# Optimization experiments

Measured on AMD Instinct MI355X. Metric: run time of the kernel, lower is better.

## Reference

```python
import jax, jax.numpy as jnp
import numpy as np

B, L, D, H = 1, 2048, 3072, 24
Dh = D // H            # 128
MLP = 4 * D            # 12288
EPS = 1e-6


def setup_inputs() -> dict:
    key = jax.random.key(0)
    ks = jax.random.split(key, 10)
    n = lambda k, shape, s=1.0: jax.random.normal(k, shape, jnp.float32) * s
    W = 0.02  # weight init scale
    return {
        "img": n(ks[0], (B, L, D)),
        "vec": n(ks[1], (B, D)),
        "pe": n(ks[2], (1, 1, L, Dh // 2, 2, 2)),
        "mod_w": n(ks[3], (D, 3 * D), W),
        "mod_b": jnp.zeros((3 * D,), jnp.float32),
        "lin1_w": n(ks[4], (D, 3 * D + MLP), W),
        "lin1_b": jnp.zeros((3 * D + MLP,), jnp.float32),
        "lin2_w": n(ks[5], (D + MLP, D), W),
        "lin2_b": jnp.zeros((D,), jnp.float32),
        "q_scale": jnp.ones((Dh,), jnp.float32),
        "k_scale": jnp.ones((Dh,), jnp.float32),
    }


def _rms_norm(x, scale):
    return x * jax.lax.rsqrt(jnp.mean(x * x, axis=-1, keepdims=True) + EPS) * scale


def _apply_rope(x, pe):
    # x: [B,H,L,Dh]; pe: [1,1,L,Dh/2,2,2]
    xr = x.reshape(*x.shape[:-1], Dh // 2, 1, 2)
    out = pe[..., 0] * xr[..., 0] + pe[..., 1] * xr[..., 1]  # [B,H,L,Dh/2,2]
    return out.reshape(*x.shape[:-1], Dh)


def reference(img, vec, pe, mod_w, mod_b, lin1_w, lin1_b, lin2_w, lin2_b, q_scale, k_scale):
    # adaLN modulation (single): shift / scale / gate, each [B,1,D]
    mod = jax.nn.silu(vec) @ mod_w + mod_b
    shift, scale, gate = jnp.split(mod[:, None, :], 3, axis=-1)

    # pre-norm LayerNorm (no affine) + modulation
    mu = jnp.mean(img, axis=-1, keepdims=True)
    var = jnp.var(img, axis=-1, keepdims=True)
    x = (1.0 + scale) * ((img - mu) * jax.lax.rsqrt(var + EPS)) + shift

    # fused QKV + MLP projection
    proj = x @ lin1_w + lin1_b                     # [B,L,3D+MLP]
    qkv, mlp = proj[..., : 3 * D], proj[..., 3 * D :]

    # 'B L (K H D) -> K B H L D'
    qkv = qkv.reshape(B, L, 3, H, Dh).transpose(2, 0, 3, 1, 4)
    q, k, v = qkv[0], qkv[1], qkv[2]

    # per-head QK RMSNorm
    q = _rms_norm(q, q_scale)
    k = _rms_norm(k, k_scale)

    # RoPE
    q = _apply_rope(q, pe)
    k = _apply_rope(k, pe)

    # attention (scale = head_dim**-0.5)
    scores = jnp.einsum("bhqd,bhkd->bhqk", q, k) * (Dh ** -0.5)
    probs = jax.nn.softmax(scores, axis=-1)
    attn = jnp.einsum("bhqk,bhkd->bhqd", probs, v)
    attn = attn.transpose(0, 2, 1, 3).reshape(B, L, D)  # 'B H L D -> B L (H D)'

    # gated parallel MLP output + residual
    out = jnp.concatenate([attn, jax.nn.gelu(mlp, approximate=True)], axis=-1) @ lin2_w + lin2_b
    return img + gate * out
```

## Files before the change

### kernel.cpp

```cpp
#include <hip/hip_runtime.h>
#include <hip/hip_bf16.h>
#include <stdint.h>


#define DEV static __device__ __forceinline__

typedef __attribute__((ext_vector_type(4))) float f32x4;
typedef __attribute__((ext_vector_type(16))) float f32x16;
typedef __attribute__((ext_vector_type(8))) short s8v;

DEV unsigned short f2bf(float f) {
  union { float f; unsigned u; } v; v.f = f;
  unsigned r = v.u + 0x7fffu + ((v.u >> 16) & 1u);
  return (unsigned short)(r >> 16);
}
DEV float bf2f(unsigned short b) {
  union { unsigned u; float f; } v; v.u = ((unsigned)b) << 16; return v.f;
}
DEV unsigned pk2bf(float a, float b) {
  union { __hip_bfloat162 h; unsigned u; } v;
  v.h = __float22bfloat162_rn(make_float2(a, b));
  return v.u;
}

DEV void gl_lds16(const void* g, void* l) {
  __builtin_amdgcn_global_load_lds(
      (const __attribute__((address_space(1))) unsigned int*)(uintptr_t)g,
      (__attribute__((address_space(3))) unsigned int*)(uint32_t)(uintptr_t)l,
      16, 0, 0);
}

__global__ __launch_bounds__(256) void modvec_partial(
    const float* __restrict__ vec, const float* __restrict__ mod_w, float* __restrict__ part) {
  __shared__ float s[384];
  const int tid = threadIdx.x;
  const int i0 = blockIdx.y * 384;
  for (int i = tid; i < 384; i += 256) {
    float v = vec[i0 + i];
    s[i] = v / (1.f + __expf(-v));
  }
  __syncthreads();
  const int j = blockIdx.x * 256 + tid;
  float acc = 0.f;
#pragma unroll 8
  for (int i = 0; i < 384; ++i) acc += s[i] * mod_w[(size_t)(i0 + i) * 9216 + j];
  part[(size_t)blockIdx.y * 9216 + j] = acc;
}

__global__ __launch_bounds__(256) void modvec_reduce(
    const float* __restrict__ part, const float* __restrict__ mod_b, float* __restrict__ mod) {
  const int j = blockIdx.x * 256 + threadIdx.x;
  float a = mod_b[j];
#pragma unroll
  for (int y = 0; y < 8; ++y) a += part[(size_t)y * 9216 + j];
  mod[j] = a;
}

__global__ __launch_bounds__(256) void ln_mod_kernel(
    const float* __restrict__ img, const float* __restrict__ mod, unsigned short* __restrict__ x) {
  const int l = blockIdx.x, tid = threadIdx.x;
  const int wave = tid >> 6;
  const f32x4* row = (const f32x4*)(img + (size_t)l * 3072);
  f32x4 v[3];
  float s = 0.f, s2 = 0.f;
#pragma unroll
  for (int i = 0; i < 3; ++i) {
    v[i] = row[tid + i * 256];
#pragma unroll
    for (int c = 0; c < 4; ++c) { s += v[i][c]; s2 += v[i][c] * v[i][c]; }
  }
#pragma unroll
  for (int m = 1; m < 64; m <<= 1) { s += __shfl_xor(s, m); s2 += __shfl_xor(s2, m); }
  __shared__ float rs[4], rs2[4];
  if ((tid & 63) == 0) { rs[wave] = s; rs2[wave] = s2; }
  __syncthreads();
  s = rs[0] + rs[1] + rs[2] + rs[3];
  s2 = rs2[0] + rs2[1] + rs2[2] + rs2[3];
  const float mu = s * (1.f / 3072.f);
  const float var = s2 * (1.f / 3072.f) - mu * mu;
  const float inv = rsqrtf(var + 1e-6f);
#pragma unroll
  for (int i = 0; i < 3; ++i) {
    int d0 = (tid + i * 256) * 4;
    unsigned out[2];
    unsigned short o[4];
#pragma unroll
    for (int c = 0; c < 4; ++c) {
      int d = d0 + c;
      float val = (1.f + mod[3072 + d]) * ((v[i][c] - mu) * inv) + mod[d];
      o[c] = f2bf(val);
    }
    out[0] = o[0] | ((unsigned)o[1] << 16);
    out[1] = o[2] | ((unsigned)o[3] << 16);
    *(uint2*)(x + (size_t)l * 3072 + d0) = make_uint2(out[0], out[1]);
  }
}

__global__ __launch_bounds__(256) void transpose_kernel(
    const float* __restrict__ W, unsigned short* __restrict__ Wt, int K, int N) {
  __shared__ float t[64][65];
  const int k0 = blockIdx.x * 64, n0 = blockIdx.y * 64;
  const int tid = threadIdx.x;
#pragma unroll
  for (int it = 0; it < 4; ++it) {
    const int k = it * 16 + (tid >> 4), c4 = (tid & 15) * 4;
    f32x4 v = *(const f32x4*)&W[(size_t)(k0 + k) * N + n0 + c4];
    t[k][c4] = v[0]; t[k][c4 + 1] = v[1]; t[k][c4 + 2] = v[2]; t[k][c4 + 3] = v[3];
  }
  __syncthreads();
#pragma unroll
  for (int it = 0; it < 2; ++it) {
    const int idx = it * 256 + tid;
    const int n = idx >> 3, k8 = (idx & 7) * 8;
    s8v o;
#pragma unroll
    for (int e = 0; e < 8; ++e) o[e] = (short)f2bf(t[k8 + e][n]);
    *(s8v*)&Wt[(size_t)(n0 + n) * K + k0 + k8] = o;
  }
}

template <int EPI>
__global__ __launch_bounds__(512, 2) void gemm256_kernel(
    const unsigned short* __restrict__ A, const unsigned short* __restrict__ Bt,
    const float* __restrict__ bias, void* __restrict__ Cout, void* __restrict__ Cout2,
    int K, int N, int nTile, int nBN) {
  __shared__ unsigned short lds[65536];
  const int tid = threadIdx.x;
  const int lane = tid & 63, w = tid >> 6;
  const int wm = w >> 2, wn = w & 3;
  const int l15 = lane & 15, l4 = lane >> 4;

  int bid = blockIdx.x;
  const int nwg = gridDim.x;
  bid = (bid & 7) * (nwg >> 3) + (bid >> 3);
  const int bz = bid / (nBN << 3);
  const int rem = bid - bz * (nBN << 3);
  const int m0 = (rem & 7) << 8;
  const int n0 = (rem >> 3) << 8;
  const int kOff = bz * nTile * 64;

  const int sr = (w << 3) + (lane >> 3);
  const int skc = ((lane & 7) ^ (sr & 7)) << 3;
  const size_t aBase = (size_t)m0 * K + kOff;
  const size_t bBase = (size_t)n0 * K + kOff;

  const int xs0 = (l4 ^ (l15 & 7)) << 3;
  const int xs1 = ((4 + l4) ^ (l15 & 7)) << 3;
  int aRow[4], bRow[2];
#pragma unroll
  for (int i = 0; i < 4; ++i) aRow[i] = (wm * 64 + i * 16 + l15) * 64;
#pragma unroll
  for (int j = 0; j < 2; ++j) bRow[j] = (wn * 32 + j * 16 + l15) * 64;

  f32x4 acc[2][2][4][2];
#pragma unroll
  for (int mq = 0; mq < 2; ++mq)
#pragma unroll
    for (int nq = 0; nq < 2; ++nq)
#pragma unroll
      for (int i = 0; i < 4; ++i)
#pragma unroll
        for (int j = 0; j < 2; ++j) acc[mq][nq][i][j] = (f32x4){0.f, 0.f, 0.f, 0.f};

#define STAGE(op, h, par, kt)                                                        \
  do {                                                                               \
    const unsigned short* _s = (op) ? Bt : A;                                        \
    const size_t _b = (op) ? bBase : aBase;                                          \
    unsigned short* _d = &lds[((par) << 15) + ((op) << 14) + ((h) << 13) + (w << 9)];\
    gl_lds16(_s + _b + (size_t)((h) * 128 + sr) * K + (kt) * 64 + skc, _d);          \
    gl_lds16(_s + _b + (size_t)((h) * 128 + 64 + sr) * K + (kt) * 64 + skc, _d + 4096);\
  } while (0)

#define FRAGP(op, h, par, rowoff, xsv) \
  (*(const s8v*)&lds[((par) << 15) + ((op) << 14) + ((h) << 13) + (rowoff) + (xsv)])

#define RD_A(dst, h, par)                                                       \
  _Pragma("unroll") for (int i = 0; i < 4; ++i) {                               \
    dst[i][0] = FRAGP(0, h, par, aRow[i], xs0);                                 \
    dst[i][1] = FRAGP(0, h, par, aRow[i], xs1);                                 \
  }

#define RD_B(dst, h, par)                                                       \
  _Pragma("unroll") for (int j = 0; j < 2; ++j) {                               \
    dst[j][0] = FRAGP(1, h, par, bRow[j], xs0);                                 \
    dst[j][1] = FRAGP(1, h, par, bRow[j], xs1);                                 \
  }

#define PH_OPEN()                                           \
  __builtin_amdgcn_s_barrier();                             \
  asm volatile("s_waitcnt lgkmcnt(0)" ::: "memory");        \
  __builtin_amdgcn_sched_barrier(0);                        \
  __builtin_amdgcn_s_setprio(1)

#define PH_CLOSE()                                          \
  __builtin_amdgcn_sched_barrier(0);                        \
  __builtin_amdgcn_s_setprio(0);                            \
  __builtin_amdgcn_s_barrier()

#define PH_CLOSE_VM(NN)                                     \
  __builtin_amdgcn_sched_barrier(0);                        \
  __builtin_amdgcn_s_setprio(0);                            \
  asm volatile("s_waitcnt vmcnt(" #NN ")" ::: "memory");    \
  __builtin_amdgcn_s_barrier()

#define MFMA_QUAD(mq, nq, av, bv)                                                      \
  _Pragma("unroll") for (int i = 0; i < 4; ++i) _Pragma("unroll") for (int j = 0; j < 2; ++j) { \
    acc[mq][nq][i][j] =                                                                \
        __builtin_amdgcn_mfma_f32_16x16x32_bf16(av[i][0], bv[j][0], acc[mq][nq][i][j], 0, 0, 0); \
    acc[mq][nq][i][j] =                                                                \
        __builtin_amdgcn_mfma_f32_16x16x32_bf16(av[i][1], bv[j][1], acc[mq][nq][i][j], 0, 0, 0); \
  }

  STAGE(0, 0, 0, 0); STAGE(1, 0, 0, 0); STAGE(1, 1, 0, 0); STAGE(0, 1, 0, 0);
  {
    const int k1 = (nTile > 1) ? 1 : 0;
    STAGE(0, 0, 1, k1); STAGE(1, 0, 1, k1); STAGE(1, 1, 1, k1);
  }
  asm volatile("s_waitcnt vmcnt(6)" ::: "memory");
  __builtin_amdgcn_s_barrier();

  s8v aA[4][2], aB[4][2], b0[2][2], b1[2][2];
  RD_A(aA, 0, 0);
  RD_B(b0, 0, 0);

#pragma unroll 2
  for (int t = 0; t < nTile; ++t) {
    const int p = t & 1, pn = p ^ 1;
    const int kt1 = (t + 1 < nTile) ? t + 1 : 0;
    const int kt2 = (t + 2 < nTile) ? t + 2 : 0;
    STAGE(0, 1, pn, kt1);
    PH_OPEN();
    RD_B(b1, 1, p);
    MFMA_QUAD(0, 0, aA, b0);
    PH_CLOSE();
    STAGE(0, 0, p, kt2);
    PH_OPEN();
    RD_A(aB, 1, p);
    MFMA_QUAD(0, 1, aA, b1);
    PH_CLOSE_VM(8);
    STAGE(1, 0, p, kt2);
    PH_OPEN();
    RD_A(aA, 0, pn);
    MFMA_QUAD(1, 0, aB, b0);
    PH_CLOSE_VM(8);
    STAGE(1, 1, p, kt2);
    PH_OPEN();
    RD_B(b0, 0, pn);
    MFMA_QUAD(1, 1, aB, b1);
    PH_CLOSE_VM(6);
  }

  asm volatile("s_waitcnt vmcnt(0) lgkmcnt(0)" ::: "memory");
  __builtin_amdgcn_s_barrier();

  if (EPI == 0) {
    if (n0 < 9216) {
#pragma unroll
      for (int mq = 0; mq < 2; ++mq)
#pragma unroll
        for (int nq = 0; nq < 2; ++nq)
#pragma unroll
          for (int j = 0; j < 2; ++j) {
            const int col = n0 + nq * 128 + wn * 32 + j * 16 + l15;
            const float bj = bias[col];
#pragma unroll
            for (int i = 0; i < 4; ++i) {
              const int row0 = m0 + mq * 128 + wm * 64 + i * 16 + (l4 << 2);
#pragma unroll
              for (int r = 0; r < 4; ++r)
                ((unsigned short*)Cout)[(size_t)(row0 + r) * 9216 + col] =
                    f2bf(acc[mq][nq][i][j][r] + bj);
            }
          }
    } else {
#pragma unroll
      for (int mq = 0; mq < 2; ++mq)
#pragma unroll
        for (int nq = 0; nq < 2; ++nq)
#pragma unroll
          for (int j = 0; j < 2; ++j) {
            const int col = n0 + nq * 128 + wn * 32 + j * 16 + l15;
            const float bj = bias[col];
#pragma unroll
            for (int i = 0; i < 4; ++i) {
              const int row0 = m0 + mq * 128 + wm * 64 + i * 16 + (l4 << 2);
#pragma unroll
              for (int r = 0; r < 4; ++r) {
                const float v = acc[mq][nq][i][j][r] + bj;
                const float y = 0.7978845608f * (v + 0.044715f * v * v * v);
                const float ex = exp2f(2.8853900818f * y);
                const float g = v - v * __builtin_amdgcn_rcpf(ex + 1.f);
                ((unsigned short*)Cout2)[(size_t)(row0 + r) * 15360 + (col - 6144)] = f2bf(g);
              }
            }
          }
    }
  } else {
#pragma unroll
    for (int mq = 0; mq < 2; ++mq)
#pragma unroll
      for (int nq = 0; nq < 2; ++nq)
#pragma unroll
        for (int j = 0; j < 2; ++j) {
          const int col = n0 + nq * 128 + wn * 32 + j * 16 + l15;
#pragma unroll
          for (int i = 0; i < 4; ++i) {
            const int row0 = m0 + mq * 128 + wm * 64 + i * 16 + (l4 << 2);
#pragma unroll
            for (int r = 0; r < 4; ++r)
              ((float*)Cout)[(size_t)bz * 2048 * N + (size_t)(row0 + r) * N + col] =
                  acc[mq][nq][i][j][r];
          }
        }
  }
#undef STAGE
#undef FRAGP
#undef RD_A
#undef RD_B
#undef PH_OPEN
#undef PH_CLOSE
#undef PH_CLOSE_VM
#undef MFMA_QUAD
}

__global__ __launch_bounds__(256) void reduce2_kernel(
    const float* __restrict__ part, const float* __restrict__ img,
    const float* __restrict__ mod, const float* __restrict__ bias, float* __restrict__ out) {
  const size_t idx = ((size_t)blockIdx.x * 256 + threadIdx.x) * 4;
  const int col = (int)(idx % 3072);
  f32x4 p0 = *(const f32x4*)(part + idx);
  f32x4 p1 = *(const f32x4*)(part + (size_t)6291456 + idx);
  f32x4 p2 = *(const f32x4*)(part + 2 * (size_t)6291456 + idx);
  f32x4 p3 = *(const f32x4*)(part + 3 * (size_t)6291456 + idx);
  f32x4 p4 = *(const f32x4*)(part + 4 * (size_t)6291456 + idx);
  f32x4 im = *(const f32x4*)(img + idx);
  f32x4 o;
#pragma unroll
  for (int e = 0; e < 4; ++e)
    o[e] = im[e] +
           mod[6144 + col + e] * (((p0[e] + p1[e]) + (p2[e] + p3[e])) + p4[e] + bias[col + e]);
  *(f32x4*)(out + idx) = o;
}

DEV void qk_one(const unsigned short* src, const float* sc, const f32x4 pe4, float extra,
                unsigned short* dst, int lane) {
  unsigned xx = *(const unsigned*)(src + 2 * lane);
  float x0 = bf2f((unsigned short)(xx & 0xffff));
  float x1 = bf2f((unsigned short)(xx >> 16));
  float ss = x0 * x0 + x1 * x1;
#pragma unroll
  for (int m = 1; m < 64; m <<= 1) ss += __shfl_xor(ss, m);
  const float inv = rsqrtf(ss * (1.f / 128.f) + 1e-6f);
  x0 *= inv * sc[2 * lane];
  x1 *= inv * sc[2 * lane + 1];
  float o0 = (pe4.x * x0 + pe4.y * x1) * extra;
  float o1 = (pe4.z * x0 + pe4.w * x1) * extra;
  *(unsigned*)(dst + 2 * lane) = (unsigned)f2bf(o0) | ((unsigned)f2bf(o1) << 16);
}

__global__ __launch_bounds__(256) void qk_prep_kernel(
    const unsigned short* __restrict__ proj, const float* __restrict__ pe,
    const float* __restrict__ q_scale, const float* __restrict__ k_scale,
    unsigned short* __restrict__ qr, unsigned short* __restrict__ kr) {
  const int l = blockIdx.x;
  const int tid = threadIdx.x, lane = tid & 63, wave = tid >> 6;
  const unsigned short* row = proj + (size_t)l * 9216;
  const f32x4 pe4 = *(const f32x4*)(pe + ((size_t)l * 64 + lane) * 4);
  const float qsc = 0.12751743761f;
#pragma unroll
  for (int hh = 0; hh < 6; ++hh) {
    const int h = wave + hh * 4;
    qk_one(row + h * 128, q_scale, pe4, qsc, qr + ((size_t)h * 2048 + l) * 128, lane);
    qk_one(row + 3072 + h * 128, k_scale, pe4, 1.f, kr + ((size_t)h * 2048 + l) * 128, lane);
  }
}

__global__ __launch_bounds__(256) void vtrans_kernel(
    const unsigned short* __restrict__ proj, unsigned short* __restrict__ vt) {
  __shared__ unsigned short t[128][136];
  const int h = blockIdx.y, l0 = blockIdx.x * 128;
  const int tid = threadIdx.x;
  const int row = tid >> 1, half = tid & 1;
  const unsigned short* src = proj + (size_t)(l0 + row) * 9216 + 6144 + h * 128 + half * 64;
#pragma unroll
  for (int cc = 0; cc < 8; ++cc)
    *(s8v*)&t[row][half * 64 + cc * 8] = *(const s8v*)(src + cc * 8);
  __syncthreads();
  const int dh = tid >> 1;
  unsigned short* dst = vt + ((size_t)h * 128 + dh) * 2048 + l0 + half * 64;
#pragma unroll
  for (int lc = 0; lc < 8; ++lc) {
    s8v o;
#pragma unroll
    for (int e = 0; e < 8; ++e) o[e] = (short)t[half * 64 + lc * 8 + e][dh];
    *(s8v*)(dst + lc * 8) = o;
  }
}

__global__ __launch_bounds__(256) void attn_kernel(
    const unsigned short* __restrict__ qr, const unsigned short* __restrict__ kr,
    const unsigned short* __restrict__ vt, unsigned short* __restrict__ A2) {
  __shared__ char lds[65536];
  const int tid = threadIdx.x, lane = tid & 63, w = tid >> 6;
  const int l31 = lane & 31, hi = lane >> 5;
  const int h = blockIdx.y;
  const int q0 = blockIdx.x * 128 + w * 32;
  const int q = q0 + l31;

  s8v qf[8];
  {
    const unsigned short* qb = qr + ((size_t)h * 2048 + q) * 128 + hi * 8;
#pragma unroll
    for (int ks = 0; ks < 8; ++ks) qf[ks] = *(const s8v*)(qb + ks * 16);
  }

  int koff[4], voff[4];
#pragma unroll
  for (int c = 0; c < 4; ++c) {
    const int ob = (w * 4 + c) * 1024 + lane * 16;
    const int row = ob >> 8;
    const int sl = (ob >> 4) & 15;
    const int ssl = sl ^ (row & 15);
    koff[c] = row * 128 + ssl * 8;
    const int dh = row * 2 + (ssl >> 3);
    voff[c] = dh * 2048 + (ssl & 7) * 8;
  }
  const unsigned short* krH = kr + (size_t)h * 2048 * 128;
  const unsigned short* vtH = vt + (size_t)h * 128 * 2048;

  f32x16 oacc[4];
#pragma unroll
  for (int rf = 0; rf < 4; ++rf)
#pragma unroll
    for (int e = 0; e < 16; ++e) oacc[rf][e] = 0.f;
  float m = -3e38f, l = 0.f;

#define ATT_STAGE(t)                                                        \
  do {                                                                      \
    char* kb_ = lds + ((t) & 1) * 32768;                                    \
    char* vb_ = kb_ + 16384;                                                \
    _Pragma("unroll") for (int c = 0; c < 4; ++c) {                         \
      gl_lds16(krH + (size_t)(t) * 8192 + koff[c], kb_ + (w * 4 + c) * 1024); \
      gl_lds16(vtH + (size_t)(t) * 64 + voff[c], vb_ + (w * 4 + c) * 1024);   \
    }                                                                       \
  } while (0)

  ATT_STAGE(0);
  __syncthreads();

  for (int t = 0; t < 32; ++t) {
    if (t + 1 < 32) ATT_STAGE(t + 1);
    char* kb = lds + (t & 1) * 32768;
    char* vb = kb + 16384;

    f32x16 st[2];
#pragma unroll
    for (int rf = 0; rf < 2; ++rf)
#pragma unroll
      for (int e = 0; e < 16; ++e) st[rf][e] = 0.f;
#pragma unroll
    for (int ks = 0; ks < 8; ++ks)
#pragma unroll
      for (int rf = 0; rf < 2; ++rf) {
        const int kvr = rf * 32 + l31;
        s8v kf = *(const s8v*)(kb + kvr * 256 + (((ks * 2 + hi) ^ (kvr & 15)) << 4));
        st[rf] = __builtin_amdgcn_mfma_f32_32x32x16_bf16(kf, qf[ks], st[rf], 0, 0, 0);
      }

    float pm = st[0][0];
#pragma unroll
    for (int rf = 0; rf < 2; ++rf)
#pragma unroll
      for (int e = 0; e < 16; ++e) pm = fmaxf(pm, st[rf][e]);
    pm = fmaxf(pm, __shfl_xor(pm, 32));
    if (__any(pm - m > 11.5f)) {
      const float mn = fmaxf(m, pm);
      const float rs = exp2f(m - mn);
      l *= rs;
#pragma unroll
      for (int rf = 0; rf < 4; ++rf)
#pragma unroll
        for (int e = 0; e < 16; ++e) oacc[rf][e] *= rs;
      m = mn;
    }
    unsigned P2[16];
#pragma unroll
    for (int rb = 0; rb < 2; ++rb)
#pragma unroll
      for (int g = 0; g < 4; ++g) {
        const float e0 = exp2f(st[rb][4 * g + 0] - m);
        const float e1 = exp2f(st[rb][4 * g + 1] - m);
        const float e2 = exp2f(st[rb][4 * g + 2] - m);
        const float e3 = exp2f(st[rb][4 * g + 3] - m);
        l += (e0 + e1) + (e2 + e3);
        P2[rb * 8 + g * 2 + 0] = pk2bf(e0, e1);
        P2[rb * 8 + g * 2 + 1] = pk2bf(e2, e3);
      }

#pragma unroll
    for (int ks = 0; ks < 4; ++ks) {
      const int iA = ((2 * ks) >> 2) * 8 + ((2 * ks) & 3) * 2;
      const int iB = ((2 * ks + 1) >> 2) * 8 + ((2 * ks + 1) & 3) * 2;
      const unsigned s0 = hi ? P2[iA] : P2[iB];
      const unsigned s1 = hi ? P2[iA + 1] : P2[iB + 1];
      const unsigned r0 = (unsigned)__shfl_xor((int)s0, 32);
      const unsigned r1 = (unsigned)__shfl_xor((int)s1, 32);
      const unsigned o0 = hi ? P2[iB] : P2[iA];
      const unsigned o1 = hi ? P2[iB + 1] : P2[iA + 1];
      union { unsigned u[4]; s8v v; } pf;
      pf.u[0] = hi ? r0 : o0;
      pf.u[1] = hi ? r1 : o1;
      pf.u[2] = hi ? o0 : r0;
      pf.u[3] = hi ? o1 : r1;
#pragma unroll
      for (int rf = 0; rf < 4; ++rf) {
        const int dh = rf * 32 + l31, r = dh >> 1;
        const int sl = ((dh & 1) << 3) + ks * 2 + hi;
        s8v vf = *(const s8v*)(vb + r * 256 + ((sl ^ (r & 15)) << 4));
        oacc[rf] = __builtin_amdgcn_mfma_f32_32x32x16_bf16(vf, pf.v, oacc[rf], 0, 0, 0);
      }
    }
    __syncthreads();
  }

  const float lf = l + __shfl_xor(l, 32);
  const float inv = 1.f / lf;
  char* ep = lds + w * 8448;
#pragma unroll
  for (int rf = 0; rf < 4; ++rf)
#pragma unroll
    for (int g = 0; g < 4; ++g) {
      const unsigned u0 = pk2bf(oacc[rf][4 * g + 0] * inv, oacc[rf][4 * g + 1] * inv);
      const unsigned u1 = pk2bf(oacc[rf][4 * g + 2] * inv, oacc[rf][4 * g + 3] * inv);
      *(uint2*)(ep + l31 * 264 + rf * 64 + g * 16 + hi * 8) = make_uint2(u0, u1);
    }
  __syncthreads();
  const int c = lane & 15, l4b = lane >> 4;
#pragma unroll
  for (int pass = 0; pass < 8; ++pass) {
    const int qq = pass * 4 + l4b;
    const uint2 a2 = *(const uint2*)(ep + qq * 264 + c * 16);
    const uint2 b2 = *(const uint2*)(ep + qq * 264 + c * 16 + 8);
    *(uint4*)(A2 + (size_t)(q0 + qq) * 15360 + h * 128 + c * 8) =
        make_uint4(a2.x, a2.y, b2.x, b2.y);
  }
#undef ATT_STAGE
}

extern "C" void kernel_launch(void* const* d_in, const int* in_sizes, int n_in,
                              void* d_out, int out_size, void* d_ws, size_t ws_size,
                              hipStream_t stream) {
  (void)in_sizes; (void)n_in; (void)out_size; (void)ws_size;
  const float* img    = (const float*)d_in[0];
  const float* vec    = (const float*)d_in[1];
  const float* pe     = (const float*)d_in[2];
  const float* mod_w  = (const float*)d_in[3];
  const float* mod_b  = (const float*)d_in[4];
  const float* lin1_w = (const float*)d_in[5];
  const float* lin1_b = (const float*)d_in[6];
  const float* lin2_w = (const float*)d_in[7];
  const float* lin2_b = (const float*)d_in[8];
  const float* q_s    = (const float*)d_in[9];
  const float* k_s    = (const float*)d_in[10];
  float* out = (float*)d_out;

  char* ws = (char*)d_ws;
  size_t off = 0;
  auto alloc = [&](size_t b) { size_t p = off; off += (b + 255) & ~(size_t)255; return p; };
  float* part          = (float*)(ws + alloc((size_t)8 * 9216 * 4));
  float* mod           = (float*)(ws + alloc((size_t)9216 * 4));
  unsigned short* x    = (unsigned short*)(ws + alloc((size_t)2048 * 3072 * 2));
  unsigned short* wT   = (unsigned short*)(ws + alloc((size_t)21504 * 3072 * 2));
  unsigned short* proj = (unsigned short*)(ws + alloc((size_t)2048 * 21504 * 2));
  unsigned short* qr   = (unsigned short*)(ws + alloc((size_t)24 * 2048 * 128 * 2));
  unsigned short* kr   = (unsigned short*)(ws + alloc((size_t)24 * 2048 * 128 * 2));
  unsigned short* vt   = (unsigned short*)(ws + alloc((size_t)24 * 128 * 2048 * 2));
  unsigned short* A2   = (unsigned short*)(ws + alloc((size_t)2048 * 15360 * 2));
  float* p2buf = (float*)proj;

  modvec_partial<<<dim3(36, 8), 256, 0, stream>>>(vec, mod_w, part);
  modvec_reduce<<<36, 256, 0, stream>>>(part, mod_b, mod);
  ln_mod_kernel<<<2048, 256, 0, stream>>>(img, mod, x);
  transpose_kernel<<<dim3(48, 336), 256, 0, stream>>>(lin1_w, wT, 3072, 21504);
  gemm256_kernel<0><<<672, 512, 0, stream>>>(x, wT, lin1_b, proj, A2, 3072, 21504, 48, 84);
  qk_prep_kernel<<<2048, 256, 0, stream>>>(proj, pe, q_s, k_s, qr, kr);
  vtrans_kernel<<<dim3(16, 24), 256, 0, stream>>>(proj, vt);
  attn_kernel<<<dim3(16, 24), 256, 0, stream>>>(qr, kr, vt, A2);
  transpose_kernel<<<dim3(240, 48), 256, 0, stream>>>(lin2_w, wT, 15360, 3072);
  gemm256_kernel<2><<<480, 512, 0, stream>>>(A2, wT, nullptr, p2buf, nullptr, 15360, 3072, 48, 12);
  reduce2_kernel<<<6144, 256, 0, stream>>>(p2buf, img, mod, lin2_b, out);
}
```

Measured before the change: 840.5 us.

## Fuse lin2 weight transpose into attention launch as extra blocks

Merges the lin2 weight transpose/bf16 conversion into the attention kernel launch by appending 11520 extra blocks that do the transpose. The attention grid is flattened from 2D to 1D. The aim is to fill idle CUs while the 384 attention blocks run and to remove one kernel launch. The risk is that transpose blocks may compete with attention for CUs and bandwidth, and the 64KB of LDS these blocks request can limit how many of them are resident.

```diff
diff --git a/kernel.cpp b/kernel.cpp
--- a/kernel.cpp
+++ b/kernel.cpp
@@ -399,12 +399,39 @@
 
 __global__ __launch_bounds__(256) void attn_kernel(
     const unsigned short* __restrict__ qr, const unsigned short* __restrict__ kr,
-    const unsigned short* __restrict__ vt, unsigned short* __restrict__ A2) {
+    const unsigned short* __restrict__ vt, unsigned short* __restrict__ A2,
+    const float* __restrict__ W2, unsigned short* __restrict__ W2t) {
   __shared__ char lds[65536];
-  const int tid = threadIdx.x, lane = tid & 63, w = tid >> 6;
+  const int bx = blockIdx.x;
+  const int tid = threadIdx.x;
+
+  if (bx >= 384) {
+    const int tb = bx - 384;
+    const int k0 = (tb % 240) * 64, n0 = (tb / 240) * 64;
+    float (*t)[65] = (float(*)[65])lds;
+#pragma unroll
+    for (int it = 0; it < 4; ++it) {
+      const int k = it * 16 + (tid >> 4), c4 = (tid & 15) * 4;
+      f32x4 v = *(const f32x4*)&W2[(size_t)(k0 + k) * 3072 + n0 + c4];
+      t[k][c4] = v[0]; t[k][c4 + 1] = v[1]; t[k][c4 + 2] = v[2]; t[k][c4 + 3] = v[3];
+    }
+    __syncthreads();
+#pragma unroll
+    for (int it = 0; it < 2; ++it) {
+      const int idx = it * 256 + tid;
+      const int n = idx >> 3, k8 = (idx & 7) * 8;
+      s8v o;
+#pragma unroll
+      for (int e = 0; e < 8; ++e) o[e] = (short)f2bf(t[k8 + e][n]);
+      *(s8v*)&W2t[(size_t)(n0 + n) * 15360 + k0 + k8] = o;
+    }
+    return;
+  }
+
+  const int lane = tid & 63, w = tid >> 6;
   const int l31 = lane & 31, hi = lane >> 5;
-  const int h = blockIdx.y;
-  const int q0 = blockIdx.x * 128 + w * 32;
+  const int h = bx >> 4;
+  const int q0 = (bx & 15) * 128 + w * 32;
   const int q = q0 + l31;
 
   s8v qf[8];
@@ -585,8 +612,7 @@
   gemm256_kernel<0><<<672, 512, 0, stream>>>(x, wT, lin1_b, proj, A2, 3072, 21504, 48, 84);
   qk_prep_kernel<<<2048, 256, 0, stream>>>(proj, pe, q_s, k_s, qr, kr);
   vtrans_kernel<<<dim3(16, 24), 256, 0, stream>>>(proj, vt);
-  attn_kernel<<<dim3(16, 24), 256, 0, stream>>>(qr, kr, vt, A2);
-  transpose_kernel<<<dim3(240, 48), 256, 0, stream>>>(lin2_w, wT, 15360, 3072);
+  attn_kernel<<<384 + 11520, 256, 0, stream>>>(qr, kr, vt, A2, lin2_w, wT);
   gemm256_kernel<2><<<480, 512, 0, stream>>>(A2, wT, nullptr, p2buf, nullptr, 15360, 3072, 48, 12);
   reduce2_kernel<<<6144, 256, 0, stream>>>(p2buf, img, mod, lin2_b, out);
 }
```

New measurement: 798.3 us. 1.05x faster.
